# Kernel optimization log

Measured on AMD Instinct MI355X. Metric: run time of the kernel, lower is better.

Reference implementation:

```python
import jax, jax.numpy as jnp
import numpy as np

ROUTING_ITERATIONS = 3


def squash(x):
    # squared norm over the capsule output dim
    sq = jnp.sum(x * x, axis=-1, keepdims=True)
    scale = sq / (1.0 + sq)
    return scale * x / jnp.sqrt(sq)


def setup_inputs() -> dict:
    key = jax.random.key(0)
    k1, k2 = jax.random.split(key)
    B, N, IN_C, K, OUT_C = 256, 1152, 8, 10, 16
    u = jax.random.normal(k1, (B, N, IN_C), dtype=jnp.float32)
    W = jax.random.normal(k2, (K, N, IN_C, OUT_C), dtype=jnp.float32)
    return {"u": u, "W": W}


def reference(u, W):
    # u: [B, N, in_c]; W: [K, N, in_c, out_c]
    # torch: u_hat = matmul(u[None,:,:,None,:], W[:,None]) -> [K, B, N, 1, out_c]
    u_hat = jnp.einsum('bni,knio->kbno', u, W)  # [K, B, N, out_c]
    b_ij = jnp.zeros_like(u_hat)
    v_j = None
    for it in range(ROUTING_ITERATIONS):
        c_ij = jax.nn.softmax(b_ij, axis=2)               # softmax over N, per out_c channel
        s_j = jnp.sum(c_ij * u_hat, axis=2, keepdims=True)  # [K, B, 1, out_c]
        v_j = squash(s_j)
        if it < ROUTING_ITERATIONS - 1:
            a_ij = jnp.sum(u_hat * v_j, axis=-1, keepdims=True)  # [K, B, N, 1]
            b_ij = b_ij + a_ij
    # match torch output shape [K, B, 1, 1, out_c]
    return v_j[:, :, :, None, :]
```

## Files before the change

kernel.cpp:

```cpp
#include <hip/hip_runtime.h>
#include <hip/hip_fp16.h>

#define Bsz 256
#define Nn  1152
#define Kk  10
#define NT  384
#define NW  6
#define S4  1160

#define W_ELEMS (Kk*Nn*128)
#define U_ELEMS (Bsz*Nn*8)

typedef _Float16 hf2_t __attribute__((ext_vector_type(2)));

static __device__ __forceinline__ unsigned pkh2(float x, float y) {
    __half2 h = __floats2half2_rn(x, y);
    return *reinterpret_cast<unsigned*>(&h);
}
static __device__ __forceinline__ float2 uph2(unsigned v) {
    __half2 h;
    *reinterpret_cast<unsigned*>(&h) = v;
    return __half22float2(h);
}
static __device__ __forceinline__ float fdot2u(unsigned a, unsigned b, float c) {
    union { unsigned u; hf2_t h; } A, B;
    A.u = a; B.u = b;
    return __builtin_amdgcn_fdot2(A.h, B.h, c, false);
}

#define PERM_LO 0x01000504u
#define PERM_HI 0x03020706u
#define ONE2    0x3C003C00u

__global__ void cvt_kernel(const float* __restrict__ W, const float* __restrict__ u,
                           __half2* __restrict__ Wh, __half2* __restrict__ uh) {
    const int idx = blockIdx.x * blockDim.x + threadIdx.x;
    const int wg = W_ELEMS / 8;
    const float4* p;
    __half2* o;
    if (idx < wg) {
        p = (const float4*)W + (size_t)idx * 2;
        o = Wh + (size_t)idx * 4;
    } else {
        const int j = idx - wg;
        p = (const float4*)u + (size_t)j * 2;
        o = uh + (size_t)j * 4;
    }
    const float4 a = p[0], b = p[1];
    o[0] = __floats2half2_rn(a.x, a.y);
    o[1] = __floats2half2_rn(a.z, a.w);
    o[2] = __floats2half2_rn(b.x, b.y);
    o[3] = __floats2half2_rn(b.z, b.w);
}

template<bool HALF>
__global__ __launch_bounds__(NT, 6)
void digitcaps_kernel(const float* __restrict__ u32, const float* __restrict__ W32,
                      const __half* __restrict__ uh, const __half* __restrict__ Wh,
                      float* __restrict__ out)
{
    const int t    = threadIdx.x;
    const int lane = t & 63;
    const int wav  = t >> 6;
    const int b    = blockIdx.x;
    const int k    = blockIdx.y;

    __shared__ unsigned       uhS[8 * S4];
    __shared__ unsigned short cS[Nn];
    __shared__ float          redS[NW * 17];
    __shared__ float          mxS[NW];

    {
        const int oh   = t & 1;
        const int nsub = t >> 1;
        for (int r = 0; r < 6; ++r) {
            const int n = r * 192 + nsub;
            float a0[8];
            #pragma unroll
            for (int o = 0; o < 8; ++o) a0[o] = 0.f;
            if (HALF) {
                const uint4 uq = *(const uint4*)(uh + ((size_t)b * Nn + n) * 8);
                const unsigned uw[4] = {uq.x, uq.y, uq.z, uq.w};
                const __half* wbase = Wh + ((size_t)(k * Nn + n)) * 128 + oh * 8;
                #pragma unroll
                for (int p = 0; p < 4; ++p) {
                    const uint4 qa = *(const uint4*)(wbase + (2 * p    ) * 16);
                    const uint4 qb = *(const uint4*)(wbase + (2 * p + 1) * 16);
                    const unsigned aw[4] = {qa.x, qa.y, qa.z, qa.w};
                    const unsigned bw[4] = {qb.x, qb.y, qb.z, qb.w};
                    #pragma unroll
                    for (int jj = 0; jj < 4; ++jj) {
                        const unsigned wl = __builtin_amdgcn_perm(aw[jj], bw[jj], PERM_LO);
                        const unsigned wh = __builtin_amdgcn_perm(aw[jj], bw[jj], PERM_HI);
                        a0[2*jj]   = fdot2u(wl, uw[p], a0[2*jj]);
                        a0[2*jj+1] = fdot2u(wh, uw[p], a0[2*jj+1]);
                    }
                }
            } else {
                float ua[8];
                const float4* up0 = (const float4*)(u32 + ((size_t)b * Nn + n) * 8);
                const float4 x0 = up0[0], x1 = up0[1];
                ua[0]=x0.x; ua[1]=x0.y; ua[2]=x0.z; ua[3]=x0.w;
                ua[4]=x1.x; ua[5]=x1.y; ua[6]=x1.z; ua[7]=x1.w;
                #pragma unroll
                for (int i = 0; i < 8; ++i) {
                    const float4* wp = (const float4*)(W32 + ((size_t)k * Nn + n) * 128) + oh * 2 + i * 4;
                    const float4 w0 = wp[0], w1 = wp[1];
                    float wv[8];
                    wv[0]=w0.x; wv[1]=w0.y; wv[2]=w0.z; wv[3]=w0.w;
                    wv[4]=w1.x; wv[5]=w1.y; wv[6]=w1.z; wv[7]=w1.w;
                    const float x = ua[i];
                    #pragma unroll
                    for (int o = 0; o < 8; ++o) a0[o] += x * wv[o];
                }
            }
            #pragma unroll
            for (int jj = 0; jj < 4; ++jj)
                uhS[(oh * 4 + jj) * S4 + n] = pkh2(a0[2*jj], a0[2*jj+1]);
        }
    }
    __syncthreads();

    float lg[3] = {0.f, 0.f, 0.f};
    unsigned vh[8];
    const int j_s = lane & 7;
    const int g_s = lane >> 3;

    for (int it = 0; it < 3; ++it) {
        if (it > 0) {
            #pragma unroll
            for (int r = 0; r < 3; ++r) {
                const int n = t + r * NT;
                float acc = 0.f;
                #pragma unroll
                for (int j = 0; j < 8; ++j)
                    acc = fdot2u(uhS[j * S4 + n], vh[j], acc);
                lg[r] += acc;
            }
            float m = fmaxf(fmaxf(lg[0], lg[1]), lg[2]);
            #pragma unroll
            for (int off = 1; off <= 32; off <<= 1)
                m = fmaxf(m, __shfl_xor(m, off));
            if (lane == 0) mxS[wav] = m;
            __syncthreads();
            float mm = mxS[0];
            #pragma unroll
            for (int w = 1; w < NW; ++w) mm = fmaxf(mm, mxS[w]);
            #pragma unroll
            for (int r = 0; r < 3; ++r) {
                const __half eh = __float2half(__expf(lg[r] - mm));
                cS[t + r * NT] = *reinterpret_cast<const unsigned short*>(&eh);
            }
            __syncthreads();
        }

        float2 sp = {0.f, 0.f};
        float dp = 0.f;
        #pragma unroll
        for (int c2 = 0; c2 < 12; ++c2) {
            const int n0 = c2 * 96 + wav * 8 + g_s;
            const int n1 = n0 + 48;
            unsigned cp;
            if (it == 0) cp = ONE2;
            else cp = (unsigned)cS[n0] | ((unsigned)cS[n1] << 16);
            const unsigned q0 = uhS[j_s * S4 + n0];
            const unsigned q1 = uhS[j_s * S4 + n1];
            const unsigned px = __builtin_amdgcn_perm(q0, q1, PERM_LO);
            const unsigned py = __builtin_amdgcn_perm(q0, q1, PERM_HI);
            sp.x = fdot2u(px, cp, sp.x);
            sp.y = fdot2u(py, cp, sp.y);
            dp   = fdot2u(cp, ONE2, dp);
        }
        #pragma unroll
        for (int off = 8; off <= 32; off <<= 1) {
            sp.x += __shfl_xor(sp.x, off);
            sp.y += __shfl_xor(sp.y, off);
            dp   += __shfl_xor(dp,   off);
        }
        if (lane < 8) {
            redS[wav * 17 + 2*j_s    ] = sp.x;
            redS[wav * 17 + 2*j_s + 1] = sp.y;
        }
        if (lane == 0) redS[wav * 17 + 16] = dp;
        __syncthreads();

        {
            const int o = lane & 15;
            float s = 0.f, d = 0.f;
            #pragma unroll
            for (int w = 0; w < NW; ++w) {
                s += redS[w * 17 + o];
                d += redS[w * 17 + 16];
            }
            s /= d;
            float s2 = s * s;
            #pragma unroll
            for (int off = 1; off <= 8; off <<= 1) s2 += __shfl_xor(s2, off);
            const float scale = (s2 / (1.f + s2)) * rsqrtf(fmaxf(s2, 1e-30f));
            const float v = s * scale;
            if (it == 2) {
                if (wav == 0 && lane < 16)
                    out[((size_t)k * Bsz + b) * 16 + lane] = v;
            } else {
                #pragma unroll
                for (int j = 0; j < 8; ++j)
                    vh[j] = pkh2(__shfl(v, 2*j), __shfl(v, 2*j + 1));
            }
        }
    }
}

extern "C" void kernel_launch(void* const* d_in, const int* in_sizes, int n_in,
                              void* d_out, int out_size, void* d_ws, size_t ws_size,
                              hipStream_t stream) {
    const float* u = (const float*)d_in[0];
    const float* W = (const float*)d_in[1];
    float* out = (float*)d_out;
    const size_t need = (size_t)(W_ELEMS + U_ELEMS) * sizeof(__half);
    if (ws_size >= need) {
        __half* Wh = (__half*)d_ws;
        __half* uh = (__half*)((char*)d_ws + (size_t)W_ELEMS * sizeof(__half));
        cvt_kernel<<<dim3((W_ELEMS + U_ELEMS) / 8 / 256), dim3(256), 0, stream>>>(
            W, u, (__half2*)Wh, (__half2*)uh);
        digitcaps_kernel<true><<<dim3(256, 10), dim3(NT), 0, stream>>>(
            nullptr, nullptr, uh, Wh, out);
    } else {
        digitcaps_kernel<false><<<dim3(256, 10), dim3(NT), 0, stream>>>(
            u, W, nullptr, nullptr, out);
    }
}
```

Measured before the change: 127.3 us.

## Use per-wave softmax max with rescaled reduction and register-resident u_hat

```diff
diff --git a/kernel.cpp b/kernel.cpp
--- a/kernel.cpp
+++ b/kernel.cpp
@@ -6,51 +6,69 @@
 #define Kk  10
 #define NT  384
 #define NW  6
-#define S4  1160
+#define S4  1156
+#define PAIRS 576
 
 #define W_ELEMS (Kk*Nn*128)
 #define U_ELEMS (Bsz*Nn*8)
+#define WCELLS  (Kk*Nn)
+#define WBLKS   (WCELLS/16)
+#define UBLKS   (U_ELEMS/8/256)
 
 typedef _Float16 hf2_t __attribute__((ext_vector_type(2)));
 
 static __device__ __forceinline__ unsigned pkh2(float x, float y) {
     __half2 h = __floats2half2_rn(x, y);
     return *reinterpret_cast<unsigned*>(&h);
-}
-static __device__ __forceinline__ float2 uph2(unsigned v) {
-    __half2 h;
-    *reinterpret_cast<unsigned*>(&h) = v;
-    return __half22float2(h);
 }
 static __device__ __forceinline__ float fdot2u(unsigned a, unsigned b, float c) {
     union { unsigned u; hf2_t h; } A, B;
     A.u = a; B.u = b;
     return __builtin_amdgcn_fdot2(A.h, B.h, c, false);
 }
+static __device__ __forceinline__ void wave_lds_fence() {
+    __builtin_amdgcn_sched_barrier(0);
+    asm volatile("s_waitcnt lgkmcnt(0)" ::: "memory");
+    __builtin_amdgcn_sched_barrier(0);
+}
 
 #define PERM_LO 0x01000504u
 #define PERM_HI 0x03020706u
 #define ONE2    0x3C003C00u
 
 __global__ void cvt_kernel(const float* __restrict__ W, const float* __restrict__ u,
-                           __half2* __restrict__ Wh, __half2* __restrict__ uh) {
-    const int idx = blockIdx.x * blockDim.x + threadIdx.x;
-    const int wg = W_ELEMS / 8;
-    const float4* p;
-    __half2* o;
-    if (idx < wg) {
-        p = (const float4*)W + (size_t)idx * 2;
-        o = Wh + (size_t)idx * 4;
+                           unsigned* __restrict__ Wh, __half2* __restrict__ uh) {
+    const int t = threadIdx.x;
+    if ((int)blockIdx.x < WBLKS) {
+        __shared__ float ws[16 * 132];
+        const size_t base = (size_t)blockIdx.x * (16 * 128);
+        const float4* p = (const float4*)(W + base) + t * 2;
+        const float4 x = p[0], y = p[1];
+        {
+            const int e = t * 8;
+            float* d = ws + (e >> 7) * 132 + (e & 127);
+            d[0]=x.x; d[1]=x.y; d[2]=x.z; d[3]=x.w;
+            d[4]=y.x; d[5]=y.y; d[6]=y.z; d[7]=y.w;
+        }
+        __syncthreads();
+        const int c = t >> 4, o = t & 15;
+        const float* s = ws + c * 132 + o;
+        uint4 r;
+        r.x = pkh2(s[0*16], s[1*16]);
+        r.y = pkh2(s[2*16], s[3*16]);
+        r.z = pkh2(s[4*16], s[5*16]);
+        r.w = pkh2(s[6*16], s[7*16]);
+        *(uint4*)(Wh + ((size_t)blockIdx.x * 16 + c) * 64 + o * 4) = r;
     } else {
-        const int j = idx - wg;
-        p = (const float4*)u + (size_t)j * 2;
-        o = uh + (size_t)j * 4;
-    }
-    const float4 a = p[0], b = p[1];
-    o[0] = __floats2half2_rn(a.x, a.y);
-    o[1] = __floats2half2_rn(a.z, a.w);
-    o[2] = __floats2half2_rn(b.x, b.y);
-    o[3] = __floats2half2_rn(b.z, b.w);
+        const int j = ((int)blockIdx.x - WBLKS) * 256 + t;
+        const float4* p = (const float4*)u + (size_t)j * 2;
+        __half2* o = uh + (size_t)j * 4;
+        const float4 a = p[0], b = p[1];
+        o[0] = __floats2half2_rn(a.x, a.y);
+        o[1] = __floats2half2_rn(a.z, a.w);
+        o[2] = __floats2half2_rn(b.x, b.y);
+        o[3] = __floats2half2_rn(b.z, b.w);
+    }
 }
 
 template<bool HALF>
@@ -65,111 +83,102 @@
     const int b    = blockIdx.x;
     const int k    = blockIdx.y;
 
-    __shared__ unsigned       uhS[8 * S4];
-    __shared__ unsigned short cS[Nn];
-    __shared__ float          redS[NW * 17];
-    __shared__ float          mxS[NW];
-
-    {
-        const int oh   = t & 1;
-        const int nsub = t >> 1;
-        for (int r = 0; r < 6; ++r) {
-            const int n = r * 192 + nsub;
-            float a0[8];
-            #pragma unroll
-            for (int o = 0; o < 8; ++o) a0[o] = 0.f;
-            if (HALF) {
-                const uint4 uq = *(const uint4*)(uh + ((size_t)b * Nn + n) * 8);
-                const unsigned uw[4] = {uq.x, uq.y, uq.z, uq.w};
-                const __half* wbase = Wh + ((size_t)(k * Nn + n)) * 128 + oh * 8;
-                #pragma unroll
-                for (int p = 0; p < 4; ++p) {
-                    const uint4 qa = *(const uint4*)(wbase + (2 * p    ) * 16);
-                    const uint4 qb = *(const uint4*)(wbase + (2 * p + 1) * 16);
-                    const unsigned aw[4] = {qa.x, qa.y, qa.z, qa.w};
-                    const unsigned bw[4] = {qb.x, qb.y, qb.z, qb.w};
-                    #pragma unroll
-                    for (int jj = 0; jj < 4; ++jj) {
-                        const unsigned wl = __builtin_amdgcn_perm(aw[jj], bw[jj], PERM_LO);
-                        const unsigned wh = __builtin_amdgcn_perm(aw[jj], bw[jj], PERM_HI);
-                        a0[2*jj]   = fdot2u(wl, uw[p], a0[2*jj]);
-                        a0[2*jj+1] = fdot2u(wh, uw[p], a0[2*jj+1]);
-                    }
-                }
-            } else {
-                float ua[8];
-                const float4* up0 = (const float4*)(u32 + ((size_t)b * Nn + n) * 8);
-                const float4 x0 = up0[0], x1 = up0[1];
-                ua[0]=x0.x; ua[1]=x0.y; ua[2]=x0.z; ua[3]=x0.w;
-                ua[4]=x1.x; ua[5]=x1.y; ua[6]=x1.z; ua[7]=x1.w;
-                #pragma unroll
-                for (int i = 0; i < 8; ++i) {
-                    const float4* wp = (const float4*)(W32 + ((size_t)k * Nn + n) * 128) + oh * 2 + i * 4;
-                    const float4 w0 = wp[0], w1 = wp[1];
-                    float wv[8];
-                    wv[0]=w0.x; wv[1]=w0.y; wv[2]=w0.z; wv[3]=w0.w;
-                    wv[4]=w1.x; wv[5]=w1.y; wv[6]=w1.z; wv[7]=w1.w;
-                    const float x = ua[i];
-                    #pragma unroll
-                    for (int o = 0; o < 8; ++o) a0[o] += x * wv[o];
-                }
-            }
-            #pragma unroll
-            for (int jj = 0; jj < 4; ++jj)
-                uhS[(oh * 4 + jj) * S4 + n] = pkh2(a0[2*jj], a0[2*jj+1]);
-        }
-    }
-    __syncthreads();
+    __shared__ unsigned uhS[8 * S4];
+    __shared__ unsigned cS2[PAIRS];
+    __shared__ float    redS[2][NW][20];
+
+    unsigned uhreg[3][8];
+
+    #pragma unroll
+    for (int r = 0; r < 3; ++r) {
+        const int n = t + r * NT;
+        float acc[16];
+        if (HALF) {
+            const uint4 uq = *(const uint4*)(uh + ((size_t)b * Nn + n) * 8);
+            const uint4* wp = (const uint4*)(Wh + ((size_t)(k * Nn + n)) * 128);
+            #pragma unroll
+            for (int o4 = 0; o4 < 4; ++o4) {
+                const uint4 w0 = wp[o4*4+0], w1 = wp[o4*4+1];
+                const uint4 w2 = wp[o4*4+2], w3 = wp[o4*4+3];
+                acc[o4*4+0] = fdot2u(w0.w, uq.w, fdot2u(w0.z, uq.z, fdot2u(w0.y, uq.y, fdot2u(w0.x, uq.x, 0.f))));
+                acc[o4*4+1] = fdot2u(w1.w, uq.w, fdot2u(w1.z, uq.z, fdot2u(w1.y, uq.y, fdot2u(w1.x, uq.x, 0.f))));
+                acc[o4*4+2] = fdot2u(w2.w, uq.w, fdot2u(w2.z, uq.z, fdot2u(w2.y, uq.y, fdot2u(w2.x, uq.x, 0.f))));
+                acc[o4*4+3] = fdot2u(w3.w, uq.w, fdot2u(w3.z, uq.z, fdot2u(w3.y, uq.y, fdot2u(w3.x, uq.x, 0.f))));
+            }
+        } else {
+            float ua[8];
+            const float4* up = (const float4*)(u32 + ((size_t)b * Nn + n) * 8);
+            const float4 x0 = up[0], x1 = up[1];
+            ua[0]=x0.x; ua[1]=x0.y; ua[2]=x0.z; ua[3]=x0.w;
+            ua[4]=x1.x; ua[5]=x1.y; ua[6]=x1.z; ua[7]=x1.w;
+            #pragma unroll
+            for (int o = 0; o < 16; ++o) acc[o] = 0.f;
+            #pragma unroll
+            for (int i = 0; i < 8; ++i) {
+                const float4* wp = (const float4*)(W32 + (((size_t)k * Nn + n) * 8 + i) * 16);
+                const float4 w0 = wp[0], w1 = wp[1], w2 = wp[2], w3 = wp[3];
+                const float x = ua[i];
+                acc[0]+=x*w0.x;  acc[1]+=x*w0.y;  acc[2]+=x*w0.z;  acc[3]+=x*w0.w;
+                acc[4]+=x*w1.x;  acc[5]+=x*w1.y;  acc[6]+=x*w1.z;  acc[7]+=x*w1.w;
+                acc[8]+=x*w2.x;  acc[9]+=x*w2.y;  acc[10]+=x*w2.z; acc[11]+=x*w2.w;
+                acc[12]+=x*w3.x; acc[13]+=x*w3.y; acc[14]+=x*w3.z; acc[15]+=x*w3.w;
+            }
+        }
+        #pragma unroll
+        for (int j = 0; j < 8; ++j) {
+            const unsigned pk = pkh2(acc[2*j], acc[2*j+1]);
+            uhreg[r][j] = pk;
+            uhS[j * S4 + n] = pk;
+        }
+    }
+    wave_lds_fence();
 
     float lg[3] = {0.f, 0.f, 0.f};
     unsigned vh[8];
     const int j_s = lane & 7;
     const int g_s = lane >> 3;
 
+    #pragma unroll
     for (int it = 0; it < 3; ++it) {
+        float m_w = 0.f;
         if (it > 0) {
             #pragma unroll
             for (int r = 0; r < 3; ++r) {
-                const int n = t + r * NT;
                 float acc = 0.f;
                 #pragma unroll
                 for (int j = 0; j < 8; ++j)
-                    acc = fdot2u(uhS[j * S4 + n], vh[j], acc);
+                    acc = fdot2u(uhreg[r][j], vh[j], acc);
                 lg[r] += acc;
             }
             float m = fmaxf(fmaxf(lg[0], lg[1]), lg[2]);
             #pragma unroll
             for (int off = 1; off <= 32; off <<= 1)
                 m = fmaxf(m, __shfl_xor(m, off));
-            if (lane == 0) mxS[wav] = m;
-            __syncthreads();
-            float mm = mxS[0];
-            #pragma unroll
-            for (int w = 1; w < NW; ++w) mm = fmaxf(mm, mxS[w]);
+            m_w = m;
             #pragma unroll
             for (int r = 0; r < 3; ++r) {
-                const __half eh = __float2half(__expf(lg[r] - mm));
-                cS[t + r * NT] = *reinterpret_cast<const unsigned short*>(&eh);
-            }
-            __syncthreads();
+                const int n = t + r * NT;
+                const __half eh = __float2half(__expf(lg[r] - m_w));
+                ((__half*)cS2)[n] = eh;
+            }
+            wave_lds_fence();
         }
 
         float2 sp = {0.f, 0.f};
         float dp = 0.f;
         #pragma unroll
-        for (int c2 = 0; c2 < 12; ++c2) {
-            const int n0 = c2 * 96 + wav * 8 + g_s;
-            const int n1 = n0 + 48;
-            unsigned cp;
-            if (it == 0) cp = ONE2;
-            else cp = (unsigned)cS[n0] | ((unsigned)cS[n1] << 16);
-            const unsigned q0 = uhS[j_s * S4 + n0];
-            const unsigned q1 = uhS[j_s * S4 + n1];
-            const unsigned px = __builtin_amdgcn_perm(q0, q1, PERM_LO);
-            const unsigned py = __builtin_amdgcn_perm(q0, q1, PERM_HI);
-            sp.x = fdot2u(px, cp, sp.x);
-            sp.y = fdot2u(py, cp, sp.y);
-            dp   = fdot2u(cp, ONE2, dp);
+        for (int r = 0; r < 3; ++r) {
+            #pragma unroll
+            for (int c = 0; c < 4; ++c) {
+                const int n0 = 64 * wav + 384 * r + 8 * g_s + 2 * c;
+                const unsigned cp = (it == 0) ? ONE2 : cS2[n0 >> 1];
+                const uint2 q = *(const uint2*)&uhS[j_s * S4 + n0];
+                const unsigned px = __builtin_amdgcn_perm(q.x, q.y, PERM_LO);
+                const unsigned py = __builtin_amdgcn_perm(q.x, q.y, PERM_HI);
+                sp.x = fdot2u(px, cp, sp.x);
+                sp.y = fdot2u(py, cp, sp.y);
+                dp   = fdot2u(cp, ONE2, dp);
+            }
         }
         #pragma unroll
         for (int off = 8; off <= 32; off <<= 1) {
@@ -177,20 +186,25 @@
             sp.y += __shfl_xor(sp.y, off);
             dp   += __shfl_xor(dp,   off);
         }
-        if (lane < 8) {
-            redS[wav * 17 + 2*j_s    ] = sp.x;
-            redS[wav * 17 + 2*j_s + 1] = sp.y;
-        }
-        if (lane == 0) redS[wav * 17 + 16] = dp;
+        const int buf = it & 1;
+        if (lane < 8)
+            *(float2*)&redS[buf][wav][2 * j_s] = make_float2(sp.x, sp.y);
+        if (lane == 0)
+            *(float2*)&redS[buf][wav][16] = make_float2(dp, m_w);
         __syncthreads();
 
-        {
+        if (it < 2 || wav == 0) {
             const int o = lane & 15;
+            float M = redS[buf][0][17];
+            #pragma unroll
+            for (int w = 1; w < NW; ++w) M = fmaxf(M, redS[buf][w][17]);
             float s = 0.f, d = 0.f;
             #pragma unroll
             for (int w = 0; w < NW; ++w) {
-                s += redS[w * 17 + o];
-                d += redS[w * 17 + 16];
+                const float2 dm = *(const float2*)&redS[buf][w][16];
+                const float sc = (it == 0) ? 1.f : __expf(dm.y - M);
+                s += sc * redS[buf][w][o];
+                d += sc * dm.x;
             }
             s /= d;
             float s2 = s * s;
@@ -220,8 +234,8 @@
     if (ws_size >= need) {
         __half* Wh = (__half*)d_ws;
         __half* uh = (__half*)((char*)d_ws + (size_t)W_ELEMS * sizeof(__half));
-        cvt_kernel<<<dim3((W_ELEMS + U_ELEMS) / 8 / 256), dim3(256), 0, stream>>>(
-            W, u, (__half2*)Wh, (__half2*)uh);
+        cvt_kernel<<<dim3(WBLKS + UBLKS), dim3(256), 0, stream>>>(
+            W, u, (unsigned*)Wh, (__half2*)uh);
         digitcaps_kernel<true><<<dim3(256, 10), dim3(NT), 0, stream>>>(
             nullptr, nullptr, uh, Wh, out);
     } else {
```

After: 200.2 us. 57.2% more time.

## Make routing softmax wave-local with per-wave max and rescaled cross-wave merge

Applied to the files above, without the earlier changes.

```diff
diff --git a/kernel.cpp b/kernel.cpp
--- a/kernel.cpp
+++ b/kernel.cpp
@@ -6,7 +6,8 @@
 #define Kk  10
 #define NT  384
 #define NW  6
-#define S4  1160
+#define S4  1156
+#define PAIRS 576
 
 #define W_ELEMS (Kk*Nn*128)
 #define U_ELEMS (Bsz*Nn*8)
@@ -16,16 +17,16 @@
 static __device__ __forceinline__ unsigned pkh2(float x, float y) {
     __half2 h = __floats2half2_rn(x, y);
     return *reinterpret_cast<unsigned*>(&h);
-}
-static __device__ __forceinline__ float2 uph2(unsigned v) {
-    __half2 h;
-    *reinterpret_cast<unsigned*>(&h) = v;
-    return __half22float2(h);
 }
 static __device__ __forceinline__ float fdot2u(unsigned a, unsigned b, float c) {
     union { unsigned u; hf2_t h; } A, B;
     A.u = a; B.u = b;
     return __builtin_amdgcn_fdot2(A.h, B.h, c, false);
+}
+static __device__ __forceinline__ void wave_lds_fence() {
+    __builtin_amdgcn_sched_barrier(0);
+    asm volatile("s_waitcnt lgkmcnt(0)" ::: "memory");
+    __builtin_amdgcn_sched_barrier(0);
 }
 
 #define PERM_LO 0x01000504u
@@ -65,16 +66,15 @@
     const int b    = blockIdx.x;
     const int k    = blockIdx.y;
 
-    __shared__ unsigned       uhS[8 * S4];
-    __shared__ unsigned short cS[Nn];
-    __shared__ float          redS[NW * 17];
-    __shared__ float          mxS[NW];
+    __shared__ unsigned uhS[8 * S4];
+    __shared__ unsigned cS2[PAIRS];
+    __shared__ float    redS[2][NW][20];
 
     {
-        const int oh   = t & 1;
-        const int nsub = t >> 1;
-        for (int r = 0; r < 6; ++r) {
-            const int n = r * 192 + nsub;
+        const int oh = lane & 1;
+        const int pr = lane >> 1;
+        for (int rr = 0; rr < 6; ++rr) {
+            const int n = 192 * rr + 32 * wav + pr;
             float a0[8];
             #pragma unroll
             for (int o = 0; o < 8; ++o) a0[o] = 0.f;
@@ -90,16 +90,16 @@
                     const unsigned bw[4] = {qb.x, qb.y, qb.z, qb.w};
                     #pragma unroll
                     for (int jj = 0; jj < 4; ++jj) {
-                        const unsigned wl = __builtin_amdgcn_perm(aw[jj], bw[jj], PERM_LO);
-                        const unsigned wh = __builtin_amdgcn_perm(aw[jj], bw[jj], PERM_HI);
-                        a0[2*jj]   = fdot2u(wl, uw[p], a0[2*jj]);
-                        a0[2*jj+1] = fdot2u(wh, uw[p], a0[2*jj+1]);
+                        const unsigned wl  = __builtin_amdgcn_perm(aw[jj], bw[jj], PERM_LO);
+                        const unsigned wh2 = __builtin_amdgcn_perm(aw[jj], bw[jj], PERM_HI);
+                        a0[2*jj]   = fdot2u(wl,  uw[p], a0[2*jj]);
+                        a0[2*jj+1] = fdot2u(wh2, uw[p], a0[2*jj+1]);
                     }
                 }
             } else {
                 float ua[8];
-                const float4* up0 = (const float4*)(u32 + ((size_t)b * Nn + n) * 8);
-                const float4 x0 = up0[0], x1 = up0[1];
+                const float4* up = (const float4*)(u32 + ((size_t)b * Nn + n) * 8);
+                const float4 x0 = up[0], x1 = up[1];
                 ua[0]=x0.x; ua[1]=x0.y; ua[2]=x0.z; ua[3]=x0.w;
                 ua[4]=x1.x; ua[5]=x1.y; ua[6]=x1.z; ua[7]=x1.w;
                 #pragma unroll
@@ -119,54 +119,52 @@
                 uhS[(oh * 4 + jj) * S4 + n] = pkh2(a0[2*jj], a0[2*jj+1]);
         }
     }
-    __syncthreads();
+    wave_lds_fence();
 
     float lg[3] = {0.f, 0.f, 0.f};
     unsigned vh[8];
     const int j_s = lane & 7;
     const int g_s = lane >> 3;
-
+    const int l5  = lane >> 5;
+    const int l31 = lane & 31;
+
+    #pragma unroll
     for (int it = 0; it < 3; ++it) {
+        float m_w = 0.f;
         if (it > 0) {
             #pragma unroll
-            for (int r = 0; r < 3; ++r) {
-                const int n = t + r * NT;
+            for (int j = 0; j < 3; ++j) {
+                const int n = 384 * j + 192 * l5 + 32 * wav + l31;
                 float acc = 0.f;
                 #pragma unroll
-                for (int j = 0; j < 8; ++j)
-                    acc = fdot2u(uhS[j * S4 + n], vh[j], acc);
-                lg[r] += acc;
+                for (int jj = 0; jj < 8; ++jj)
+                    acc = fdot2u(uhS[jj * S4 + n], vh[jj], acc);
+                lg[j] += acc;
             }
             float m = fmaxf(fmaxf(lg[0], lg[1]), lg[2]);
             #pragma unroll
             for (int off = 1; off <= 32; off <<= 1)
                 m = fmaxf(m, __shfl_xor(m, off));
-            if (lane == 0) mxS[wav] = m;
-            __syncthreads();
-            float mm = mxS[0];
-            #pragma unroll
-            for (int w = 1; w < NW; ++w) mm = fmaxf(mm, mxS[w]);
-            #pragma unroll
-            for (int r = 0; r < 3; ++r) {
-                const __half eh = __float2half(__expf(lg[r] - mm));
-                cS[t + r * NT] = *reinterpret_cast<const unsigned short*>(&eh);
-            }
-            __syncthreads();
+            m_w = m;
+            #pragma unroll
+            for (int j = 0; j < 3; ++j) {
+                const int n = 384 * j + 192 * l5 + 32 * wav + l31;
+                const __half eh = __float2half(__expf(lg[j] - m_w));
+                ((__half*)cS2)[n] = eh;
+            }
+            wave_lds_fence();
         }
 
         float2 sp = {0.f, 0.f};
         float dp = 0.f;
         #pragma unroll
-        for (int c2 = 0; c2 < 12; ++c2) {
-            const int n0 = c2 * 96 + wav * 8 + g_s;
-            const int n1 = n0 + 48;
-            unsigned cp;
-            if (it == 0) cp = ONE2;
-            else cp = (unsigned)cS[n0] | ((unsigned)cS[n1] << 16);
-            const unsigned q0 = uhS[j_s * S4 + n0];
-            const unsigned q1 = uhS[j_s * S4 + n1];
-            const unsigned px = __builtin_amdgcn_perm(q0, q1, PERM_LO);
-            const unsigned py = __builtin_amdgcn_perm(q0, q1, PERM_HI);
+        for (int cc = 0; cc < 12; ++cc) {
+            const int P  = g_s + 8 * cc;
+            const int n0 = 192 * (P >> 4) + 32 * wav + 2 * (P & 15);
+            const unsigned cp = (it == 0) ? ONE2 : cS2[n0 >> 1];
+            const uint2 q = *(const uint2*)&uhS[j_s * S4 + n0];
+            const unsigned px = __builtin_amdgcn_perm(q.x, q.y, PERM_LO);
+            const unsigned py = __builtin_amdgcn_perm(q.x, q.y, PERM_HI);
             sp.x = fdot2u(px, cp, sp.x);
             sp.y = fdot2u(py, cp, sp.y);
             dp   = fdot2u(cp, ONE2, dp);
@@ -177,20 +175,25 @@
             sp.y += __shfl_xor(sp.y, off);
             dp   += __shfl_xor(dp,   off);
         }
-        if (lane < 8) {
-            redS[wav * 17 + 2*j_s    ] = sp.x;
-            redS[wav * 17 + 2*j_s + 1] = sp.y;
-        }
-        if (lane == 0) redS[wav * 17 + 16] = dp;
+        const int buf = it & 1;
+        if (lane < 8)
+            *(float2*)&redS[buf][wav][2 * j_s] = make_float2(sp.x, sp.y);
+        if (lane == 0)
+            *(float2*)&redS[buf][wav][16] = make_float2(dp, m_w);
         __syncthreads();
 
-        {
+        if (it < 2 || wav == 0) {
             const int o = lane & 15;
+            float M = redS[buf][0][17];
+            #pragma unroll
+            for (int w = 1; w < NW; ++w) M = fmaxf(M, redS[buf][w][17]);
             float s = 0.f, d = 0.f;
             #pragma unroll
             for (int w = 0; w < NW; ++w) {
-                s += redS[w * 17 + o];
-                d += redS[w * 17 + 16];
+                const float2 dm = *(const float2*)&redS[buf][w][16];
+                const float sc = (it == 0) ? 1.f : __expf(dm.y - M);
+                s += sc * redS[buf][w][o];
+                d += sc * dm.x;
             }
             s /= d;
             float s2 = s * s;
```

Measured after the change: 124.8 us. 2.0% less time.
